# Kernel tuning notes

Hardware: AMD Instinct MI355X
Metric: run time of the kernel (lower is better)

The kernel has to match this reference:

```python
import jax, jax.numpy as jnp
import numpy as np

BEV_RANGE = 50.0
LAMBDA_PROGRESS = 1.0
LAMBDA_COLLISION = 2.0
LAMBDA_COMFORT = 0.5


def _mlp2(x, w1, b1, w2, b2):
    # Linear -> ReLU -> Linear ; weights stored as (in, out)
    h = jax.nn.relu(x @ w1 + b1)
    return h @ w2 + b2


def setup_inputs() -> dict:
    key = jax.random.key(0)
    ks = jax.random.split(key, 12)
    B, K, T = 32, 64, 80
    C, H, W = 256, 200, 200
    s = 0.02
    return {
        "trajectories": jax.random.normal(ks[0], (B, K, T, 2), jnp.float32) * 10.0,
        "goals": jax.random.normal(ks[1], (B, K, 2), jnp.float32) * 10.0,
        "bev_features": jax.random.normal(ks[2], (B, C, H, W), jnp.float32),
        # feature_extractor: Linear(2,64) -> ReLU -> Linear(64,128) -> ReLU
        "fe_w1": jax.random.normal(ks[3], (2, 64), jnp.float32) * s,
        "fe_b1": jnp.zeros((64,), jnp.float32),
        "fe_w2": jax.random.normal(ks[4], (64, 128), jnp.float32) * s,
        "fe_b2": jnp.zeros((128,), jnp.float32),
        # collision_head: Linear(128+C,64) -> ReLU -> Linear(64,1)
        "ch_w1": jax.random.normal(ks[5], (128 + C, 64), jnp.float32) * s,
        "ch_b1": jnp.zeros((64,), jnp.float32),
        "ch_w2": jax.random.normal(ks[6], (64, 1), jnp.float32) * s,
        "ch_b2": jnp.zeros((1,), jnp.float32),
    }


def reference(trajectories, goals, bev_features, fe_w1, fe_b1, fe_w2, fe_b2,
              ch_w1, ch_b1, ch_w2, ch_b2):
    B, K, T, _ = trajectories.shape
    C, H, W = bev_features.shape[1:]

    # ---- progress score: 1 / (1 + ||final - goal||) -> (B, K)
    final_pos = trajectories[:, :, -1, :]
    dist = jnp.linalg.norm(final_pos - goals, axis=-1)
    progress = 1.0 / (1.0 + dist)

    # ---- collision score -> (B, K)
    # grid index computation (truncation toward zero, like torch .long())
    gx = ((trajectories[..., 0] / BEV_RANGE + 1.0) * W / 2.0).astype(jnp.int32)
    gy = ((trajectories[..., 1] / BEV_RANGE + 1.0) * H / 2.0).astype(jnp.int32)
    gx = jnp.clip(gx, 0, W - 1)
    gy = jnp.clip(gy, 0, H - 1)
    grid_flat = (gy * W + gx).reshape(B, K * T)            # (B, K*T)

    bev_flat = bev_features.reshape(B, C, H * W).transpose(0, 2, 1)  # (B, HW, C)
    # batched irregular gather: per-sample lookup of trajectory cells
    bev_at_traj = jax.vmap(lambda bf, idx: bf[idx])(bev_flat, grid_flat)
    bev_at_traj = bev_at_traj.reshape(B, K, T, C)
    bev_avg = bev_at_traj.mean(axis=2)                     # (B, K, C)

    # trajectory MLP features (extractor ends with ReLU)
    traj_feat = jax.nn.relu(_mlp2(trajectories, fe_w1, fe_b1, fe_w2, fe_b2))
    traj_avg = traj_feat.mean(axis=2)                      # (B, K, 128)

    combined = jnp.concatenate([traj_avg, bev_avg], axis=-1)
    logit = _mlp2(combined, ch_w1, ch_b1, ch_w2, ch_b2)[..., 0]
    collision = jax.nn.sigmoid(logit)

    # ---- comfort score -> (B, K)
    vel = trajectories[:, :, 1:, :] - trajectories[:, :, :-1, :]
    acc = vel[:, :, 1:, :] - vel[:, :, :-1, :]
    mean_acc = jnp.linalg.norm(acc, axis=-1).mean(axis=-1)
    comfort = 1.0 / (1.0 + mean_acc)

    scores = (LAMBDA_PROGRESS * progress
              - LAMBDA_COLLISION * collision
              + LAMBDA_COMFORT * comfort)
    return scores, progress, collision, comfort
```

## Files before the change

kernel.cpp:

```cpp
#include <hip/hip_runtime.h>
#include <cstdint>
#include <cstddef>

constexpr int NB = 32;
constexpr int NK = 64;
constexpr int NT = 80;
constexpr int NC = 256;
constexpr int NH = 200;
constexpr int NW = 200;
constexpr int NHW = NH * NW;
constexpr int NBK = NB * NK;
constexpr int NWORDS = NHW / 32;
constexpr int CAP = 4096;

typedef __attribute__((ext_vector_type(8))) short bf16x8;
typedef __attribute__((ext_vector_type(4))) float f32x4;

__device__ inline unsigned short f2bf(float f) {
    unsigned u = __builtin_bit_cast(unsigned, f);
    return (unsigned short)((u + 0x7fffu + ((u >> 16) & 1u)) >> 16);
}

__global__ __launch_bounds__(512) void dedup_kernel(
    const float* __restrict__ traj,
    unsigned short* __restrict__ ws_rank,
    unsigned short* __restrict__ ws_list,
    int* __restrict__ ws_ncell)
{
    const int b = blockIdx.x;
    const int tid = threadIdx.x;

    __shared__ unsigned int bitmap[NWORDS];
    __shared__ unsigned short cells[NK * NT];
    __shared__ int word_pref[NWORDS];
    __shared__ int wave_sums[8];

    for (int i = tid; i < NWORDS; i += 512) bitmap[i] = 0u;
    __syncthreads();

    const float* tb = traj + (size_t)b * NK * NT * 2;
    for (int p = tid; p < NK * NT; p += 512) {
        float x = tb[2 * p];
        float y = tb[2 * p + 1];
        int gx = (int)((x / 50.0f + 1.0f) * 100.0f);
        int gy = (int)((y / 50.0f + 1.0f) * 100.0f);
        gx = min(max(gx, 0), NW - 1);
        gy = min(max(gy, 0), NH - 1);
        int cell = gy * NW + gx;
        int k = p / NT, t = p - k * NT;
        cells[t * NK + k] = (unsigned short)cell;
        atomicOr(&bitmap[cell >> 5], 1u << (cell & 31));
    }
    __syncthreads();

    const int base_w = tid * 3;
    int cnts[3];
    int local = 0;
    #pragma unroll
    for (int j = 0; j < 3; ++j) {
        int w = base_w + j;
        int c = (w < NWORDS) ? __popc(bitmap[w]) : 0;
        cnts[j] = c;
        local += c;
    }
    const int lane = tid & 63, wv = tid >> 6;
    int incl = local;
    #pragma unroll
    for (int off = 1; off < 64; off <<= 1) {
        int v = __shfl_up(incl, off);
        if (lane >= off) incl += v;
    }
    if (lane == 63) wave_sums[wv] = incl;
    __syncthreads();
    int wbase = 0;
    for (int i = 0; i < wv; ++i) wbase += wave_sums[i];
    const int excl = wbase + incl - local;

    int run = excl;
    #pragma unroll
    for (int j = 0; j < 3; ++j) {
        int w = base_w + j;
        if (w < NWORDS) {
            word_pref[w] = run;
            unsigned int bits = bitmap[w];
            int r = run;
            while (bits) {
                int bit = __ffs(bits) - 1;
                bits &= bits - 1;
                if (r < CAP) ws_list[b * CAP + r] = (unsigned short)(w * 32 + bit);
                ++r;
            }
            run += cnts[j];
        }
    }
    if (tid == 511) ws_ncell[b] = min(excl + local, CAP);
    __syncthreads();

    unsigned short* rb = ws_rank + (size_t)b * NT * NK;
    for (int i = tid; i < NK * NT; i += 512) {
        int cell = cells[i];
        unsigned int word = bitmap[cell >> 5];
        int rank = word_pref[cell >> 5] + __popc(word & ((1u << (cell & 31)) - 1u));
        rb[i] = (unsigned short)min(rank, CAP - 1);
    }
}

__global__ __launch_bounds__(256) void gather_kernel(
    const float* __restrict__ bev,
    const unsigned short* __restrict__ ws_rank,
    const unsigned short* __restrict__ ws_list,
    const int* __restrict__ ws_ncell,
    float* __restrict__ ws_bev)
{
    const int blk = blockIdx.x;
    const int b = blk >> 8;
    const int c = blk & 255;
    const int tid = threadIdx.x;

    __shared__ float vals[CAP];

    const float* plane = bev + ((size_t)b * NC + c) * NHW;
    const int n = ws_ncell[b];
    const unsigned short* lst = ws_list + b * CAP;

    for (int u = tid; u < n; u += 256) vals[u] = plane[lst[u]];
    __syncthreads();

    const int k = tid >> 2, l = tid & 3;
    const unsigned short* rb = ws_rank + (size_t)b * NT * NK;
    float s = 0.0f;
    #pragma unroll
    for (int i = 0; i < 20; ++i) {
        const int t = l + 4 * i;
        s += vals[rb[t * NK + k]];
    }
    s += __shfl_xor(s, 1);
    s += __shfl_xor(s, 2);
    if (l == 0) ws_bev[((size_t)b * NC + c) * NK + k] = s * (1.0f / 80.0f);
}

__global__ __launch_bounds__(128) void mlp_kernel(
    const float* __restrict__ traj, const float* __restrict__ goals,
    const float* __restrict__ fe_w1, const float* __restrict__ fe_b1,
    const float* __restrict__ fe_w2, const float* __restrict__ fe_b2,
    const float* __restrict__ ch_w1, const float* __restrict__ ch_b1,
    const float* __restrict__ ch_w2, const float* __restrict__ ch_b2,
    const float* __restrict__ ws_bev, float* __restrict__ out)
{
    const int bk = blockIdx.x;
    const int b = bk >> 6, k = bk & 63;
    const int tid = threadIdx.x;
    const int lane = tid & 63, wv = tid >> 6;

    __shared__ float tr[NT * 2];
    __shared__ unsigned short hS[NT * 64];
    __shared__ unsigned short w2S[128 * 64];
    __shared__ float comb[384];
    __shared__ float accn_s[NT - 2];
    __shared__ float sh_pc[2];
    __shared__ float sh_head;

    const float* tp = traj + (size_t)bk * (NT * 2);
    for (int i = tid; i < NT * 2; i += 128) tr[i] = tp[i];
    __syncthreads();

    {
        const int il = lane & 15;
        const int jg = (lane >> 4) & 3;
        #pragma unroll
        for (int ii = 0; ii < 8; ++ii) {
            int i = il + 16 * ii;
            #pragma unroll
            for (int jj = 0; jj < 4; ++jj) {
                int jp = jg + 4 * (wv * 4 + jj);
                int j0 = 2 * jp;
                float lo = fe_w2[(size_t)j0 * 128 + i];
                float hi = fe_w2[(size_t)(j0 + 1) * 128 + i];
                unsigned pack = (unsigned)f2bf(lo) | ((unsigned)f2bf(hi) << 16);
                int off = i * 128 + ((jp * 4) ^ ((i & 7) << 4));
                *(unsigned*)((char*)w2S + off) = pack;
            }
        }
    }
    #pragma unroll
    for (int it = 0; it < 20; ++it) {
        int u = tid + 128 * it;
        int t = u >> 5, jp = u & 31;
        float x = tr[2 * t], y = tr[2 * t + 1];
        int j0 = 2 * jp;
        float h0 = fmaxf(x * fe_w1[j0]     + y * fe_w1[64 + j0]     + fe_b1[j0],     0.f);
        float h1 = fmaxf(x * fe_w1[j0 + 1] + y * fe_w1[64 + j0 + 1] + fe_b1[j0 + 1], 0.f);
        unsigned pack = (unsigned)f2bf(h0) | ((unsigned)f2bf(h1) << 16);
        int off = t * 128 + ((jp * 4) ^ ((t & 7) << 4));
        *(unsigned*)((char*)hS + off) = pack;
    }
    if (tid < NT - 2) {
        float ax = tr[2 * (tid + 2)]     - 2.0f * tr[2 * (tid + 1)]     + tr[2 * tid];
        float ay = tr[2 * (tid + 2) + 1] - 2.0f * tr[2 * (tid + 1) + 1] + tr[2 * tid + 1];
        accn_s[tid] = sqrtf(ax * ax + ay * ay);
    }
    comb[128 + tid]       = ws_bev[((size_t)b * NC + tid) * NK + k];
    comb[256 + tid]       = ws_bev[((size_t)b * NC + tid + 128) * NK + k];
    __syncthreads();

    {
        const int cl = lane & 15;
        const int kg = (lane >> 4) & 3;
        bf16x8 bfr[4][2];
        float b2v[4];
        #pragma unroll
        for (int nn = 0; nn < 4; ++nn) {
            int col = wv * 64 + nn * 16 + cl;
            b2v[nn] = fe_b2[col];
            #pragma unroll
            for (int s = 0; s < 2; ++s) {
                int off = col * 128 + ((s * 64 + kg * 16) ^ ((col & 7) << 4));
                bfr[nn][s] = *(const bf16x8*)((const char*)w2S + off);
            }
        }
        float cs[4] = {0.f, 0.f, 0.f, 0.f};
        #pragma unroll
        for (int m = 0; m < 5; ++m) {
            int row = m * 16 + cl;
            bf16x8 a0 = *(const bf16x8*)((const char*)hS + row * 128 + ((kg * 16)      ^ ((row & 7) << 4)));
            bf16x8 a1 = *(const bf16x8*)((const char*)hS + row * 128 + ((64 + kg * 16) ^ ((row & 7) << 4)));
            #pragma unroll
            for (int nn = 0; nn < 4; ++nn) {
                f32x4 acc = {0.f, 0.f, 0.f, 0.f};
                acc = __builtin_amdgcn_mfma_f32_16x16x32_bf16(a0, bfr[nn][0], acc, 0, 0, 0);
                acc = __builtin_amdgcn_mfma_f32_16x16x32_bf16(a1, bfr[nn][1], acc, 0, 0, 0);
                #pragma unroll
                for (int r = 0; r < 4; ++r) cs[nn] += fmaxf(acc[r] + b2v[nn], 0.f);
            }
        }
        #pragma unroll
        for (int nn = 0; nn < 4; ++nn) {
            cs[nn] += __shfl_xor(cs[nn], 16);
            cs[nn] += __shfl_xor(cs[nn], 32);
            if (lane < 16) comb[wv * 64 + nn * 16 + lane] = cs[nn] * (1.0f / 80.0f);
        }
    }
    __syncthreads();

    if (tid < 64) {
        float a = ch_b1[tid];
        for (int m = 0; m < 384; ++m) a += comb[m] * ch_w1[m * 64 + tid];
        float v = fmaxf(a, 0.0f) * ch_w2[tid];
        #pragma unroll
        for (int off = 32; off >= 1; off >>= 1) v += __shfl_xor(v, off);
        if (tid == 0) sh_head = v;
    } else {
        int j = tid - 64;
        float a = (j < NT - 2) ? accn_s[j] : 0.0f;
        if (j < NT - 2 - 64) a += accn_s[j + 64];
        #pragma unroll
        for (int off = 32; off >= 1; off >>= 1) a += __shfl_xor(a, off);
        if (j == 0) {
            float mean_acc = a / (float)(NT - 2);
            sh_pc[1] = 1.0f / (1.0f + mean_acc);
            float fx = tr[2 * (NT - 1)], fy = tr[2 * (NT - 1) + 1];
            float dx = fx - goals[bk * 2], dy = fy - goals[bk * 2 + 1];
            sh_pc[0] = 1.0f / (1.0f + sqrtf(dx * dx + dy * dy));
        }
    }
    __syncthreads();

    if (tid == 0) {
        float logit = sh_head + ch_b2[0];
        float collision = 1.0f / (1.0f + expf(-logit));
        float progress = sh_pc[0], comfort = sh_pc[1];
        out[bk]           = progress - 2.0f * collision + 0.5f * comfort;
        out[NBK + bk]     = progress;
        out[2 * NBK + bk] = collision;
        out[3 * NBK + bk] = comfort;
    }
}

extern "C" void kernel_launch(void* const* d_in, const int* in_sizes, int n_in,
                              void* d_out, int out_size, void* d_ws, size_t ws_size,
                              hipStream_t stream)
{
    const float* traj  = (const float*)d_in[0];
    const float* goals = (const float*)d_in[1];
    const float* bev   = (const float*)d_in[2];
    const float* fe_w1 = (const float*)d_in[3];
    const float* fe_b1 = (const float*)d_in[4];
    const float* fe_w2 = (const float*)d_in[5];
    const float* fe_b2 = (const float*)d_in[6];
    const float* ch_w1 = (const float*)d_in[7];
    const float* ch_b1 = (const float*)d_in[8];
    const float* ch_w2 = (const float*)d_in[9];
    const float* ch_b2 = (const float*)d_in[10];
    float* out = (float*)d_out;

    unsigned short* ws_rank  = (unsigned short*)d_ws;
    unsigned short* ws_list  = (unsigned short*)((char*)d_ws + (size_t)NB * NT * NK * 2);
    int*            ws_ncell = (int*)((char*)ws_list + (size_t)NB * CAP * 2);
    float*          ws_bev   = (float*)((char*)ws_ncell + 128);

    dedup_kernel<<<NB, 512, 0, stream>>>(traj, ws_rank, ws_list, ws_ncell);
    gather_kernel<<<NB * NC, 256, 0, stream>>>(bev, ws_rank, ws_list, ws_ncell, ws_bev);
    mlp_kernel<<<NBK, 128, 0, stream>>>(traj, goals, fe_w1, fe_b1, fe_w2, fe_b2,
                                        ch_w1, ch_b1, ch_w2, ch_b2, ws_bev, out);
}
```

Before: 132.8 us.

## Prepack fe_w2 fragments once, widen dedup, batch gather loads, split head GEMV

Adds a small kernel that converts fe_w2 to bf16 MFMA fragment layout once, so each of the 2048 MLP blocks loads fragments directly instead of repacking the weight into LDS. The dedup kernel now runs with 1024 threads. The gather kernel issues 16 index and value loads up front per thread to increase memory-level parallelism, at the cost of clamped redundant loads when the cell count is small. The collision-head GEMV is split across both waves and combined through shared memory. These changes add an extra kernel launch and more registers in the gather kernel.

```diff
diff --git a/kernel.cpp b/kernel.cpp
--- a/kernel.cpp
+++ b/kernel.cpp
@@ -21,7 +21,26 @@
     return (unsigned short)((u + 0x7fffu + ((u >> 16) & 1u)) >> 16);
 }
 
-__global__ __launch_bounds__(512) void dedup_kernel(
+__global__ __launch_bounds__(256) void w2pack_kernel(
+    const float* __restrict__ fe_w2, unsigned* __restrict__ ws_w2f)
+{
+    const int g = blockIdx.x * 256 + threadIdx.x;
+    const int lane = g & 63, fid = g >> 6;
+    const int s = fid & 1, nn = (fid >> 1) & 3, wv = fid >> 3;
+    const int cl = lane & 15, kg = lane >> 4;
+    const int col = wv * 64 + nn * 16 + cl;
+    unsigned pk[4];
+    #pragma unroll
+    for (int p = 0; p < 4; ++p) {
+        int j = s * 32 + kg * 8 + 2 * p;
+        unsigned lo = f2bf(fe_w2[(size_t)j * 128 + col]);
+        unsigned hi = f2bf(fe_w2[(size_t)(j + 1) * 128 + col]);
+        pk[p] = lo | (hi << 16);
+    }
+    *(uint4*)(ws_w2f + (size_t)g * 4) = make_uint4(pk[0], pk[1], pk[2], pk[3]);
+}
+
+__global__ __launch_bounds__(1024) void dedup_kernel(
     const float* __restrict__ traj,
     unsigned short* __restrict__ ws_rank,
     unsigned short* __restrict__ ws_list,
@@ -33,13 +52,13 @@
     __shared__ unsigned int bitmap[NWORDS];
     __shared__ unsigned short cells[NK * NT];
     __shared__ int word_pref[NWORDS];
-    __shared__ int wave_sums[8];
-
-    for (int i = tid; i < NWORDS; i += 512) bitmap[i] = 0u;
+    __shared__ int wave_sums[16];
+
+    for (int i = tid; i < NWORDS; i += 1024) bitmap[i] = 0u;
     __syncthreads();
 
     const float* tb = traj + (size_t)b * NK * NT * 2;
-    for (int p = tid; p < NK * NT; p += 512) {
+    for (int p = tid; p < NK * NT; p += 1024) {
         float x = tb[2 * p];
         float y = tb[2 * p + 1];
         int gx = (int)((x / 50.0f + 1.0f) * 100.0f);
@@ -53,11 +72,11 @@
     }
     __syncthreads();
 
-    const int base_w = tid * 3;
-    int cnts[3];
+    const int base_w = tid * 2;
+    int cnts[2];
     int local = 0;
     #pragma unroll
-    for (int j = 0; j < 3; ++j) {
+    for (int j = 0; j < 2; ++j) {
         int w = base_w + j;
         int c = (w < NWORDS) ? __popc(bitmap[w]) : 0;
         cnts[j] = c;
@@ -78,7 +97,7 @@
 
     int run = excl;
     #pragma unroll
-    for (int j = 0; j < 3; ++j) {
+    for (int j = 0; j < 2; ++j) {
         int w = base_w + j;
         if (w < NWORDS) {
             word_pref[w] = run;
@@ -93,11 +112,11 @@
             run += cnts[j];
         }
     }
-    if (tid == 511) ws_ncell[b] = min(excl + local, CAP);
+    if (tid == 1023) ws_ncell[b] = min(excl + local, CAP);
     __syncthreads();
 
     unsigned short* rb = ws_rank + (size_t)b * NT * NK;
-    for (int i = tid; i < NK * NT; i += 512) {
+    for (int i = tid; i < NK * NT; i += 1024) {
         int cell = cells[i];
         unsigned int word = bitmap[cell >> 5];
         int rank = word_pref[cell >> 5] + __popc(word & ((1u << (cell & 31)) - 1u));
@@ -123,7 +142,17 @@
     const int n = ws_ncell[b];
     const unsigned short* lst = ws_list + b * CAP;
 
-    for (int u = tid; u < n; u += 256) vals[u] = plane[lst[u]];
+    unsigned short li[16];
+    #pragma unroll
+    for (int it = 0; it < 16; ++it)
+        li[it] = lst[min(tid + (it << 8), n - 1)];
+    float rv[16];
+    #pragma unroll
+    for (int it = 0; it < 16; ++it)
+        rv[it] = plane[li[it]];
+    #pragma unroll
+    for (int it = 0; it < 16; ++it)
+        vals[min(tid + (it << 8), n - 1)] = rv[it];
     __syncthreads();
 
     const int k = tid >> 2, l = tid & 3;
@@ -142,9 +171,10 @@
 __global__ __launch_bounds__(128) void mlp_kernel(
     const float* __restrict__ traj, const float* __restrict__ goals,
     const float* __restrict__ fe_w1, const float* __restrict__ fe_b1,
-    const float* __restrict__ fe_w2, const float* __restrict__ fe_b2,
+    const float* __restrict__ fe_b2,
     const float* __restrict__ ch_w1, const float* __restrict__ ch_b1,
     const float* __restrict__ ch_w2, const float* __restrict__ ch_b2,
+    const unsigned* __restrict__ ws_w2f,
     const float* __restrict__ ws_bev, float* __restrict__ out)
 {
     const int bk = blockIdx.x;
@@ -154,34 +184,15 @@
 
     __shared__ float tr[NT * 2];
     __shared__ unsigned short hS[NT * 64];
-    __shared__ unsigned short w2S[128 * 64];
     __shared__ float comb[384];
     __shared__ float accn_s[NT - 2];
     __shared__ float sh_pc[2];
-    __shared__ float sh_head;
+    __shared__ float sh_part[64];
 
     const float* tp = traj + (size_t)bk * (NT * 2);
     for (int i = tid; i < NT * 2; i += 128) tr[i] = tp[i];
     __syncthreads();
 
-    {
-        const int il = lane & 15;
-        const int jg = (lane >> 4) & 3;
-        #pragma unroll
-        for (int ii = 0; ii < 8; ++ii) {
-            int i = il + 16 * ii;
-            #pragma unroll
-            for (int jj = 0; jj < 4; ++jj) {
-                int jp = jg + 4 * (wv * 4 + jj);
-                int j0 = 2 * jp;
-                float lo = fe_w2[(size_t)j0 * 128 + i];
-                float hi = fe_w2[(size_t)(j0 + 1) * 128 + i];
-                unsigned pack = (unsigned)f2bf(lo) | ((unsigned)f2bf(hi) << 16);
-                int off = i * 128 + ((jp * 4) ^ ((i & 7) << 4));
-                *(unsigned*)((char*)w2S + off) = pack;
-            }
-        }
-    }
     #pragma unroll
     for (int it = 0; it < 20; ++it) {
         int u = tid + 128 * it;
@@ -199,8 +210,8 @@
         float ay = tr[2 * (tid + 2) + 1] - 2.0f * tr[2 * (tid + 1) + 1] + tr[2 * tid + 1];
         accn_s[tid] = sqrtf(ax * ax + ay * ay);
     }
-    comb[128 + tid]       = ws_bev[((size_t)b * NC + tid) * NK + k];
-    comb[256 + tid]       = ws_bev[((size_t)b * NC + tid + 128) * NK + k];
+    comb[128 + tid] = ws_bev[((size_t)b * NC + tid) * NK + k];
+    comb[256 + tid] = ws_bev[((size_t)b * NC + tid + 128) * NK + k];
     __syncthreads();
 
     {
@@ -210,12 +221,11 @@
         float b2v[4];
         #pragma unroll
         for (int nn = 0; nn < 4; ++nn) {
-            int col = wv * 64 + nn * 16 + cl;
-            b2v[nn] = fe_b2[col];
+            b2v[nn] = fe_b2[wv * 64 + nn * 16 + cl];
             #pragma unroll
             for (int s = 0; s < 2; ++s) {
-                int off = col * 128 + ((s * 64 + kg * 16) ^ ((col & 7) << 4));
-                bfr[nn][s] = *(const bf16x8*)((const char*)w2S + off);
+                int g = (wv * 8 + nn * 2 + s) * 64 + lane;
+                bfr[nn][s] = *(const bf16x8*)(ws_w2f + (size_t)g * 4);
             }
         }
         float cs[4] = {0.f, 0.f, 0.f, 0.f};
@@ -242,37 +252,42 @@
     }
     __syncthreads();
 
-    if (tid < 64) {
-        float a = ch_b1[tid];
-        for (int m = 0; m < 384; ++m) a += comb[m] * ch_w1[m * 64 + tid];
-        float v = fmaxf(a, 0.0f) * ch_w2[tid];
-        #pragma unroll
-        for (int off = 32; off >= 1; off >>= 1) v += __shfl_xor(v, off);
-        if (tid == 0) sh_head = v;
+    float a_part;
+    if (wv == 0) {
+        a_part = ch_b1[lane];
+        for (int m = 0; m < 192; ++m) a_part += comb[m] * ch_w1[m * 64 + lane];
     } else {
-        int j = tid - 64;
-        float a = (j < NT - 2) ? accn_s[j] : 0.0f;
-        if (j < NT - 2 - 64) a += accn_s[j + 64];
-        #pragma unroll
-        for (int off = 32; off >= 1; off >>= 1) a += __shfl_xor(a, off);
-        if (j == 0) {
-            float mean_acc = a / (float)(NT - 2);
+        float s = accn_s[lane];
+        if (lane < NT - 2 - 64) s += accn_s[lane + 64];
+        #pragma unroll
+        for (int off = 32; off >= 1; off >>= 1) s += __shfl_xor(s, off);
+        if (lane == 0) {
+            float mean_acc = s / (float)(NT - 2);
             sh_pc[1] = 1.0f / (1.0f + mean_acc);
             float fx = tr[2 * (NT - 1)], fy = tr[2 * (NT - 1) + 1];
             float dx = fx - goals[bk * 2], dy = fy - goals[bk * 2 + 1];
             sh_pc[0] = 1.0f / (1.0f + sqrtf(dx * dx + dy * dy));
         }
-    }
-    __syncthreads();
-
-    if (tid == 0) {
-        float logit = sh_head + ch_b2[0];
-        float collision = 1.0f / (1.0f + expf(-logit));
-        float progress = sh_pc[0], comfort = sh_pc[1];
-        out[bk]           = progress - 2.0f * collision + 0.5f * comfort;
-        out[NBK + bk]     = progress;
-        out[2 * NBK + bk] = collision;
-        out[3 * NBK + bk] = comfort;
+        a_part = 0.f;
+        for (int m = 192; m < 384; ++m) a_part += comb[m] * ch_w1[m * 64 + lane];
+        sh_part[lane] = a_part;
+    }
+    __syncthreads();
+
+    if (wv == 0) {
+        float a = a_part + sh_part[lane];
+        float v = fmaxf(a, 0.0f) * ch_w2[lane];
+        #pragma unroll
+        for (int off = 32; off >= 1; off >>= 1) v += __shfl_xor(v, off);
+        if (lane == 0) {
+            float logit = v + ch_b2[0];
+            float collision = 1.0f / (1.0f + expf(-logit));
+            float progress = sh_pc[0], comfort = sh_pc[1];
+            out[bk]           = progress - 2.0f * collision + 0.5f * comfort;
+            out[NBK + bk]     = progress;
+            out[2 * NBK + bk] = collision;
+            out[3 * NBK + bk] = comfort;
+        }
     }
 }
 
@@ -294,12 +309,14 @@
     float* out = (float*)d_out;
 
     unsigned short* ws_rank  = (unsigned short*)d_ws;
-    unsigned short* ws_list  = (unsigned short*)((char*)d_ws + (size_t)NB * NT * NK * 2);
-    int*            ws_ncell = (int*)((char*)ws_list + (size_t)NB * CAP * 2);
+    unsigned short* ws_list  = ws_rank + (size_t)NB * NT * NK;
+    int*            ws_ncell = (int*)(ws_list + (size_t)NB * CAP);
     float*          ws_bev   = (float*)((char*)ws_ncell + 128);
-
-    dedup_kernel<<<NB, 512, 0, stream>>>(traj, ws_rank, ws_list, ws_ncell);
+    unsigned*       ws_w2f   = (unsigned*)(ws_bev + (size_t)NB * NC * NK);
+
+    w2pack_kernel<<<4, 256, 0, stream>>>(fe_w2, ws_w2f);
+    dedup_kernel<<<NB, 1024, 0, stream>>>(traj, ws_rank, ws_list, ws_ncell);
     gather_kernel<<<NB * NC, 256, 0, stream>>>(bev, ws_rank, ws_list, ws_ncell, ws_bev);
-    mlp_kernel<<<NBK, 128, 0, stream>>>(traj, goals, fe_w1, fe_b1, fe_w2, fe_b2,
-                                        ch_w1, ch_b1, ch_w2, ch_b2, ws_bev, out);
-}
+    mlp_kernel<<<NBK, 128, 0, stream>>>(traj, goals, fe_w1, fe_b1, fe_b2,
+                                        ch_w1, ch_b1, ch_w2, ch_b2, ws_w2f, ws_bev, out);
+}
```

Result: faster. 114.9 us (-13.5%).
